# Performance work log

Measured on AMD Instinct MI355X. Metric: run time of the kernel, lower is better.

The kernel has to match this reference:

```python
import jax, jax.numpy as jnp
import numpy as np
from jax import lax

DIM = 384
NUM_HEADS = 6
STRIDE_Q = 1
STRIDE_KV = 2
BN_EPS = 1e-5
SCALE = DIM ** (-0.5)  # CvT scales by dim_out, not head_dim


def setup_inputs() -> dict:
    key = jax.random.key(0)
    ks = jax.random.split(key, 8)
    B, H, W, C = 32, 28, 28, DIM
    T = 1 + H * W
    x = jax.random.normal(ks[0], (B, T, C), dtype=jnp.float32)
    conv_w = jax.random.normal(ks[1], (3, C, 1, 3, 3), dtype=jnp.float32) * 0.1
    bn_gamma = jnp.ones((3, C), dtype=jnp.float32)
    bn_beta = jnp.zeros((3, C), dtype=jnp.float32)
    bn_mean = jnp.zeros((3, C), dtype=jnp.float32)
    bn_var = jnp.ones((3, C), dtype=jnp.float32)
    w_q = jax.random.normal(ks[2], (C, C), dtype=jnp.float32) * 0.02
    w_k = jax.random.normal(ks[3], (C, C), dtype=jnp.float32) * 0.02
    w_v = jax.random.normal(ks[4], (C, C), dtype=jnp.float32) * 0.02
    w_proj = jax.random.normal(ks[5], (C, C), dtype=jnp.float32) * 0.02
    b_proj = jnp.zeros((C,), dtype=jnp.float32)
    return {"x": x, "conv_w": conv_w, "bn_gamma": bn_gamma, "bn_beta": bn_beta,
            "bn_mean": bn_mean, "bn_var": bn_var, "w_q": w_q, "w_k": w_k,
            "w_v": w_v, "w_proj": w_proj, "b_proj": b_proj, "h": H, "w": W}


def _dw_conv_bn(x_sp, cw, gamma, beta, mean, var, stride):
    # x_sp: [B, C, H, W]; cw: [C, 1, 3, 3] depthwise (groups=C); inference BN
    C = x_sp.shape[1]
    y = lax.conv_general_dilated(
        x_sp, cw, window_strides=(stride, stride), padding=((1, 1), (1, 1)),
        feature_group_count=C, dimension_numbers=("NCHW", "OIHW", "NCHW"))
    inv = gamma * lax.rsqrt(var + BN_EPS)
    y = y * inv[None, :, None, None] + (beta - mean * inv)[None, :, None, None]
    B, Cc, Hc, Wc = y.shape
    return y.reshape(B, Cc, Hc * Wc).transpose(0, 2, 1)  # b (h w) c


def reference(x, conv_w, bn_gamma, bn_beta, bn_mean, bn_var,
              w_q, w_k, w_v, w_proj, b_proj, h, w):
    B, T, C = x.shape
    nh, hd = NUM_HEADS, C // NUM_HEADS
    cls_tok, x_tok = x[:, :1], x[:, 1:]
    x_sp = x_tok.reshape(B, h, w, C).transpose(0, 3, 1, 2)  # b c h w

    q = _dw_conv_bn(x_sp, conv_w[0], bn_gamma[0], bn_beta[0], bn_mean[0], bn_var[0], STRIDE_Q)
    k = _dw_conv_bn(x_sp, conv_w[1], bn_gamma[1], bn_beta[1], bn_mean[1], bn_var[1], STRIDE_KV)
    v = _dw_conv_bn(x_sp, conv_w[2], bn_gamma[2], bn_beta[2], bn_mean[2], bn_var[2], STRIDE_KV)

    q = jnp.concatenate([cls_tok, q], axis=1)
    k = jnp.concatenate([cls_tok, k], axis=1)
    v = jnp.concatenate([cls_tok, v], axis=1)

    def split_heads(t, wm):  # linear proj then b t (h d) -> b h t d
        t = t @ wm.T
        Bt, Tt, _ = t.shape
        return t.reshape(Bt, Tt, nh, hd).transpose(0, 2, 1, 3)

    q = split_heads(q, w_q)
    k = split_heads(k, w_k)
    v = split_heads(v, w_v)

    attn = jax.nn.softmax(jnp.einsum("bhld,bhtd->bhlt", q, k) * SCALE, axis=-1)
    out = jnp.einsum("bhlt,bhtd->bhld", attn, v)
    out = out.transpose(0, 2, 1, 3).reshape(B, -1, C)  # b t (h d)
    return out @ w_proj.T + b_proj
```

## Files before the change

kernel.cpp:

```cpp
#include <hip/hip_runtime.h>
#include <math.h>

#define B_SZ   32
#define C_DIM  384
#define H_IN   28
#define W_IN   28
#define TQ     785
#define TKV    197
#define NH     6
#define HD     64
#define SCALE_F 0.05103103630798287f
#define SCALE_L2E (0.05103103630798287f * 1.4426950408889634f)
#define BN_EPS_F 1e-5f

#define QROWS    25120
#define KVROWS   6304
#define QROWS_P  25344
#define KVROWS_P 6528
#define WELEM    147456
#define VT_LD    208

#define QT256    99
#define KVT256   25

typedef _Float16 f16;
typedef f16  f16x8 __attribute__((ext_vector_type(8)));
typedef f16  f16x4 __attribute__((ext_vector_type(4)));
typedef float f32x4 __attribute__((ext_vector_type(4)));

__device__ __forceinline__ void split16(float v, f16& h, f16& l) {
    h = (f16)v;
    l = (f16)(v - (float)h);
}

__device__ __forceinline__ void cp16(void* lds, const void* g) {
    __builtin_amdgcn_global_load_lds(
        (const __attribute__((address_space(1))) unsigned int*)g,
        (__attribute__((address_space(3))) unsigned int*)lds, 16, 0, 0);
}

__device__ __forceinline__ bool swz(int id, int yMax, int& y, int& n0) {
    int g = id / 24, w = id - g * 24;
    y = g * 8 + (w & 7);
    n0 = (w >> 3) * 128;
    return y < yMax;
}

__global__ __launch_bounds__(256) void prep_kernel(
    const float* __restrict__ wq, const float* __restrict__ wk,
    const float* __restrict__ wv, const float* __restrict__ wp,
    const float* __restrict__ conv_w,
    const float* __restrict__ gamma, const float* __restrict__ beta,
    const float* __restrict__ mean, const float* __restrict__ var,
    f16* __restrict__ Wh, f16* __restrict__ Wl,
    float* __restrict__ wAll)
{
    int idx = blockIdx.x * 256 + threadIdx.x;
    if (idx < 4 * WELEM) {
        int which = idx / WELEM, rem = idx - which * WELEM;
        const float* s = (which == 0) ? wq : (which == 1) ? wk : (which == 2) ? wv : wp;
        float v = s[rem];
        if (which == 0) v *= SCALE_L2E;
        f16 h, l;
        split16(v, h, l);
        Wh[idx] = h; Wl[idx] = l;
    } else if (idx < 4 * WELEM + 3 * C_DIM) {
        int k = idx - 4 * WELEM;
        int cv = k / C_DIM, c = k - cv * C_DIM;
        float inv = gamma[k] * rsqrtf(var[k] + BN_EPS_F);
#pragma unroll
        for (int t = 0; t < 9; ++t)
            wAll[cv * 3840 + t * C_DIM + c] = conv_w[(size_t)cv * C_DIM * 9 + c * 9 + t] * inv;
        wAll[cv * 3840 + 9 * C_DIM + c] = beta[k] - mean[k] * inv;
    }
}

__global__ __launch_bounds__(256) void fused_conv_kernel(
    const float* __restrict__ x,
    const float* __restrict__ wAll,
    f16* __restrict__ q, f16* __restrict__ k, f16* __restrict__ v)
{
    __shared__ float sW[3 * 3840];
    int tid = threadIdx.x;
    int b = blockIdx.x, oi = blockIdx.y;

    if (oi == H_IN) {
        if (tid < 96) {
            int c = tid * 4;
            float4 vv = *(const float4*)&x[(size_t)b * TQ * C_DIM + c];
            float a[4] = {vv.x, vv.y, vv.z, vv.w};
            f16x4 hv;
#pragma unroll
            for (int u = 0; u < 4; ++u) hv[u] = (f16)a[u];
            size_t oq = (size_t)b * TQ * C_DIM + c;
            size_t okv = (size_t)b * TKV * C_DIM + c;
            *(f16x4*)&q[oq] = hv;
            *(f16x4*)&k[okv] = hv;
            *(f16x4*)&v[okv] = hv;
        }
        return;
    }

#pragma unroll
    for (int i = 0; i < 12; ++i) {
        int idx = tid + 256 * i;
        if (idx < 2880) cp16(&sW[idx * 4], &wAll[idx * 4]);
    }
    __syncthreads();

    const size_t xb = (size_t)b * TQ * C_DIM + C_DIM;
    bool oi_even = (oi & 1) == 0;

    for (int it = 0; it < 11; ++it) {
        int idx = tid + 256 * it;
        if (idx >= 28 * 96) break;
        int oj = idx / 96, cg = idx - oj * 96;
        int c = cg * 4;

        float4 xv[9];
#pragma unroll
        for (int di = 0; di < 3; ++di) {
            int ii = oi + di - 1;
            bool rok = (ii >= 0) && (ii < H_IN);
#pragma unroll
            for (int dj = 0; dj < 3; ++dj) {
                int jj = oj + dj - 1;
                bool ok = rok && (jj >= 0) && (jj < W_IN);
                xv[di * 3 + dj] = ok ? *(const float4*)&x[xb + ((size_t)ii * W_IN + jj) * C_DIM + c]
                                     : make_float4(0.f, 0.f, 0.f, 0.f);
            }
        }

        {
            float4 acc = *(const float4*)&sW[0 * 3840 + 9 * C_DIM + c];
#pragma unroll
            for (int t = 0; t < 9; ++t) {
                float4 w4 = *(const float4*)&sW[0 * 3840 + t * C_DIM + c];
                acc.x += w4.x * xv[t].x; acc.y += w4.y * xv[t].y;
                acc.z += w4.z * xv[t].z; acc.w += w4.w * xv[t].w;
            }
            f16x4 hv;
            hv[0] = (f16)acc.x; hv[1] = (f16)acc.y; hv[2] = (f16)acc.z; hv[3] = (f16)acc.w;
            size_t off = ((size_t)b * TQ + 1 + oi * W_IN + oj) * C_DIM + c;
            *(f16x4*)&q[off] = hv;
        }

        if (oi_even && ((oj & 1) == 0)) {
            int p = (oi >> 1) * 14 + (oj >> 1);
            size_t off = ((size_t)b * TKV + 1 + p) * C_DIM + c;
#pragma unroll
            for (int cv = 1; cv <= 2; ++cv) {
                float4 acc = *(const float4*)&sW[cv * 3840 + 9 * C_DIM + c];
#pragma unroll
                for (int t = 0; t < 9; ++t) {
                    float4 w4 = *(const float4*)&sW[cv * 3840 + t * C_DIM + c];
                    acc.x += w4.x * xv[t].x; acc.y += w4.y * xv[t].y;
                    acc.z += w4.z * xv[t].z; acc.w += w4.w * xv[t].w;
                }
                f16x4 hv;
                hv[0] = (f16)acc.x; hv[1] = (f16)acc.y; hv[2] = (f16)acc.z; hv[3] = (f16)acc.w;
                if (cv == 1) *(f16x4*)&k[off] = hv;
                else         *(f16x4*)&v[off] = hv;
            }
        }
    }
}

__device__ __forceinline__ void gemm_body_s(
    const f16* __restrict__ Ah,
    const f16* __restrict__ Wh, const f16* __restrict__ Wl,
    const float* __restrict__ bias,
    float* __restrict__ Cf, f16* __restrict__ Co,
    int M, int mode, int m0, int n0)
{
    __shared__ f16 lds[3 * 16384];

    const int t = threadIdx.x;
    const int wv = t >> 6, lane = t & 63;
    const int wr = (wv >> 1) * 64;
    const int wc = (wv & 1) * 64;
    const int lrow = lane & 15, quad = lane >> 4;
    const int qsw = quad ^ ((lrow >> 1) & 3);

    const int sr = t >> 2;
    const int g  = (t & 3) ^ ((t >> 3) & 3);

    const f16* gA0 = Ah + (size_t)(m0 + sr) * 384 + g * 8;
    const f16* gA1 = gA0 + 128 * 384;
    const f16* gBh = Wh + (size_t)(n0 + sr) * 384 + g * 8;
    const f16* gBl = Wl + (size_t)(n0 + sr) * 384 + g * 8;

#define STAGE_S(buf, kk) do {                                 \
        f16* d = lds + (buf) * 16384 + t * 8;                 \
        const int ko = (kk) * 32;                             \
        cp16(d,         gA0 + ko);                            \
        cp16(d + 4096,  gA1 + ko);                            \
        cp16(d + 8192,  gBh + ko);                            \
        cp16(d + 12288, gBl + ko);                            \
    } while (0)

    f32x4 acc[4][4];
#pragma unroll
    for (int i = 0; i < 4; ++i)
#pragma unroll
        for (int j = 0; j < 4; ++j)
            acc[i][j] = (f32x4){0.f, 0.f, 0.f, 0.f};

    STAGE_S(0, 0);
    STAGE_S(1, 1);

#pragma unroll
    for (int kk = 0; kk < 12; ++kk) {
        if (kk == 11) asm volatile("s_waitcnt vmcnt(0)" ::: "memory");
        else          asm volatile("s_waitcnt vmcnt(4)" ::: "memory");
        __builtin_amdgcn_s_barrier();
        __builtin_amdgcn_sched_barrier(0);

        if (kk < 10) {
            STAGE_S((kk + 2) % 3, kk + 2);
            __builtin_amdgcn_sched_barrier(0);
        }

        const f16* bp = lds + (kk % 3) * 16384;
        f16x8 ah[4], bh[4], bl[4];
#pragma unroll
        for (int i = 0; i < 4; ++i) {
            int ro = (wr + i * 16 + lrow) * 32 + qsw * 8;
            ah[i] = *(const f16x8*)&bp[ro];
        }
#pragma unroll
        for (int j = 0; j < 4; ++j) {
            int ro = (wc + j * 16 + lrow) * 32 + qsw * 8;
            bh[j] = *(const f16x8*)&bp[8192 + ro];
            bl[j] = *(const f16x8*)&bp[12288 + ro];
        }
        asm volatile("s_waitcnt lgkmcnt(0)" ::: "memory");
        __builtin_amdgcn_sched_barrier(0);

        __builtin_amdgcn_s_setprio(1);
#pragma unroll
        for (int i = 0; i < 4; ++i)
#pragma unroll
            for (int j = 0; j < 4; ++j) {
                acc[i][j] = __builtin_amdgcn_mfma_f32_16x16x32_f16(ah[i], bh[j], acc[i][j], 0, 0, 0);
                acc[i][j] = __builtin_amdgcn_mfma_f32_16x16x32_f16(ah[i], bl[j], acc[i][j], 0, 0, 0);
            }
        __builtin_amdgcn_s_setprio(0);
    }
#undef STAGE_S

#pragma unroll
    for (int i = 0; i < 4; ++i) {
        int grow0 = m0 + wr + i * 16 + quad * 4;
#pragma unroll
        for (int j = 0; j < 4; ++j) {
            int gcol = n0 + wc + j * 16 + lrow;
            float bb = (bias && mode == 0) ? bias[gcol] : 0.f;
#pragma unroll
            for (int r = 0; r < 4; ++r) {
                int grow = grow0 + r;
                if (grow >= M) continue;
                float vv = acc[i][j][r] + bb;
                if (mode == 0) {
                    Cf[(size_t)grow * 384 + gcol] = vv;
                } else if (mode == 1) {
                    Co[(size_t)grow * 384 + gcol] = (f16)vv;
                } else {
                    int bb2 = grow / TKV;
                    int key = grow - bb2 * TKV;
                    size_t off = (size_t)bb2 * 384 * VT_LD + (size_t)gcol * VT_LD + key;
                    Co[off] = (f16)vv;
                }
            }
        }
    }
}

__global__ __launch_bounds__(512, 2) void qkv_proj_kernel(
    const f16* __restrict__ q, const f16* __restrict__ k, const f16* __restrict__ v,
    const f16* __restrict__ Wh, const f16* __restrict__ Wl,
    f16* __restrict__ Qp, f16* __restrict__ Kp, f16* __restrict__ VT,
    int yMax)
{
    int y, n0;
    if (!swz(blockIdx.x, yMax, y, n0)) return;
    if (y < QT256)
        gemm_body_s(q, Wh, Wl, nullptr, nullptr, Qp, QROWS, 1, y * 256, n0);
    else if (y < QT256 + KVT256)
        gemm_body_s(k, Wh + WELEM, Wl + WELEM, nullptr, nullptr, Kp,
                    KVROWS, 1, (y - QT256) * 256, n0);
    else
        gemm_body_s(v, Wh + 2 * WELEM, Wl + 2 * WELEM, nullptr, nullptr, VT,
                    KVROWS, 2, (y - QT256 - KVT256) * 256, n0);
}

__global__ __launch_bounds__(512, 2) void v_proj_kernel(
    const f16* __restrict__ v,
    const f16* __restrict__ Wh, const f16* __restrict__ Wl,
    f16* __restrict__ VT)
{
    int y, n0;
    if (!swz(blockIdx.x, KVT256, y, n0)) return;
    gemm_body_s(v, Wh, Wl, nullptr, nullptr, VT, KVROWS, 2, y * 256, n0);
}

__global__ __launch_bounds__(512, 2) void out_proj_kernel(
    const f16* __restrict__ Ah,
    const f16* __restrict__ Wh, const f16* __restrict__ Wl,
    const float* __restrict__ bias, float* __restrict__ Cf)
{
    int y, n0;
    if (!swz(blockIdx.x, QT256, y, n0)) return;
    gemm_body_s(Ah, Wh, Wl, bias, Cf, nullptr, QROWS, 0, y * 256, n0);
}

__global__ __launch_bounds__(256) void attn_mfma8(
    const f16* __restrict__ Qp, const f16* __restrict__ Kp,
    const f16* __restrict__ VT, f16* __restrict__ Oh)
{
    __shared__ f16 sQ[2][64][32];
    __shared__ f16 sKa[2][64][32];
    __shared__ f16 sKb[2][64][32];
    __shared__ float sPs[64][68];

    int t = threadIdx.x;
    int wv = t >> 6, lane = t & 63;
    int c = lane & 15, quad = lane >> 4;
    int wq0 = wv * 16;

    int L = blockIdx.x;
    int xcd = L & 7, s_ = L >> 3;
    int pg = s_ / 13, tt = s_ - pg * 13;
    int panel = pg * 8 + xcd;
    int b = panel / NH, h = panel - b * NH;
    int q0 = tt * 64;

    const size_t qbase  = (size_t)b * TQ * C_DIM + h * HD;
    const size_t kbase  = (size_t)b * TKV * C_DIM + h * HD;
    const size_t vtbase = (size_t)b * 384 * VT_LD + (size_t)h * HD * VT_LD;

#define STAGE_T(DST, EXPR) do {                                      \
        _Pragma("unroll") for (int i = 0; i < 2; ++i) {              \
            int idx = t + 256 * i;                                   \
            int ks = idx >> 8, row = (idx >> 2) & 63, sg = (idx & 3) * 8; \
            cp16(&DST[ks][row][sg], (EXPR));                         \
        } } while (0)

#define QK(KT, BUF) do {                                             \
        __builtin_amdgcn_s_setprio(1);                               \
        _Pragma("unroll") for (int ks = 0; ks < 2; ++ks) {           \
            _Pragma("unroll") for (int j = 0; j < 4; ++j) {          \
                f16x8 k8 = *(const f16x8*)&BUF[ks][j * 16 + c][quad * 8]; \
                s[KT][j] = __builtin_amdgcn_mfma_f32_16x16x32_f16(q8[ks], k8, s[KT][j], 0, 0, 0); \
            } }                                                      \
        __builtin_amdgcn_s_setprio(0);                               \
    } while (0)

    f32x4 s[4][4];
#pragma unroll
    for (int kt = 0; kt < 4; ++kt)
#pragma unroll
        for (int j = 0; j < 4; ++j)
            s[kt][j] = (f32x4){0.f, 0.f, 0.f, 0.f};

    STAGE_T(sQ,  &Qp[qbase + (size_t)(q0 + row) * C_DIM + ks * 32 + sg]);
    STAGE_T(sKa, &Kp[kbase + (size_t)(0 * 64 + row) * C_DIM + ks * 32 + sg]);
    __syncthreads();

    f16x8 q8[2];
#pragma unroll
    for (int ks = 0; ks < 2; ++ks)
        q8[ks] = *(const f16x8*)&sQ[ks][wq0 + c][quad * 8];

    STAGE_T(sKb, &Kp[kbase + (size_t)(1 * 64 + row) * C_DIM + ks * 32 + sg]);
    QK(0, sKa);
    __syncthreads();
    STAGE_T(sKa, &Kp[kbase + (size_t)(2 * 64 + row) * C_DIM + ks * 32 + sg]);
    QK(1, sKb);
    __syncthreads();
    STAGE_T(sKb, &Kp[kbase + (size_t)(3 * 64 + row) * C_DIM + ks * 32 + sg]);
    QK(2, sKa);
    __syncthreads();
    QK(3, sKb);
    __syncthreads();

    STAGE_T(sKa, &VT[vtbase + (size_t)row * VT_LD + 0 * 64 + ks * 32 + sg]);
    STAGE_T(sKb, &VT[vtbase + (size_t)row * VT_LD + 1 * 64 + ks * 32 + sg]);

#pragma unroll
    for (int r = 0; r < 4; ++r) {
        s[3][0][r] = (c < 5) ? s[3][0][r] : -1e30f;
        s[3][1][r] = -1e30f;
        s[3][2][r] = -1e30f;
        s[3][3][r] = -1e30f;
    }

    float inv_r[4];
#pragma unroll
    for (int r = 0; r < 4; ++r) {
        float mx = -1e30f;
#pragma unroll
        for (int kt = 0; kt < 4; ++kt)
#pragma unroll
            for (int j = 0; j < 4; ++j)
                mx = fmaxf(mx, s[kt][j][r]);
        mx = fmaxf(mx, __shfl_xor(mx, 1));
        mx = fmaxf(mx, __shfl_xor(mx, 2));
        mx = fmaxf(mx, __shfl_xor(mx, 4));
        mx = fmaxf(mx, __shfl_xor(mx, 8));
        float sum = 0.f;
#pragma unroll
        for (int kt = 0; kt < 4; ++kt)
#pragma unroll
            for (int j = 0; j < 4; ++j) {
                float pv = exp2f(s[kt][j][r] - mx);
                s[kt][j][r] = pv;
                sum += pv;
            }
        sum += __shfl_xor(sum, 1);
        sum += __shfl_xor(sum, 2);
        sum += __shfl_xor(sum, 4);
        sum += __shfl_xor(sum, 8);
        inv_r[r] = 1.f / sum;
    }

    f32x4 o[4];
#pragma unroll
    for (int j = 0; j < 4; ++j) o[j] = (f32x4){0.f, 0.f, 0.f, 0.f};

#define SPS_WRITE(VTI) do {                                          \
        _Pragma("unroll") for (int r = 0; r < 4; ++r)                \
            _Pragma("unroll") for (int j = 0; j < 4; ++j)            \
                sPs[wq0 + quad * 4 + r][j * 16 + c] = s[VTI][j][r];  \
    } while (0)

#define PV(BUF) do {                                                 \
        _Pragma("unroll") for (int ks = 0; ks < 2; ++ks) {           \
            float4 p0 = *(const float4*)&sPs[wq0 + c][ks * 32 + quad * 8]; \
            float4 p1 = *(const float4*)&sPs[wq0 + c][ks * 32 + quad * 8 + 4]; \
            f16x8 p8;                                                \
            p8[0] = (f16)p0.x; p8[1] = (f16)p0.y; p8[2] = (f16)p0.z; p8[3] = (f16)p0.w; \
            p8[4] = (f16)p1.x; p8[5] = (f16)p1.y; p8[6] = (f16)p1.z; p8[7] = (f16)p1.w; \
            __builtin_amdgcn_s_setprio(1);                           \
            _Pragma("unroll") for (int j = 0; j < 4; ++j) {          \
                f16x8 v8 = *(const f16x8*)&BUF[ks][j * 16 + c][quad * 8]; \
                o[j] = __builtin_amdgcn_mfma_f32_16x16x32_f16(p8, v8, o[j], 0, 0, 0); \
            }                                                        \
            __builtin_amdgcn_s_setprio(0);                           \
        } } while (0)

    __syncthreads();
    SPS_WRITE(0);
    PV(sKa);
    __syncthreads();
    STAGE_T(sKa, &VT[vtbase + (size_t)row * VT_LD + 2 * 64 + ks * 32 + sg]);
    SPS_WRITE(1);
    PV(sKb);
    __syncthreads();
    STAGE_T(sKb, &VT[vtbase + (size_t)row * VT_LD + 3 * 64 + ks * 32 + sg]);
    SPS_WRITE(2);
    PV(sKa);
    __syncthreads();
    SPS_WRITE(3);
    PV(sKb);

#pragma unroll
    for (int r = 0; r < 4; ++r) {
        int gq = q0 + wq0 + quad * 4 + r;
        if (gq >= TQ) continue;
        float inv = inv_r[r];
#pragma unroll
        for (int j = 0; j < 4; ++j) {
            size_t off = (size_t)(b * TQ + gq) * C_DIM + h * HD + j * 16 + c;
            Oh[off] = (f16)(o[j][r] * inv);
        }
    }
#undef STAGE_T
#undef QK
#undef SPS_WRITE
#undef PV
}

extern "C" void kernel_launch(void* const* d_in, const int* in_sizes, int n_in,
                              void* d_out, int out_size, void* d_ws, size_t ws_size,
                              hipStream_t stream) {
    const float* x       = (const float*)d_in[0];
    const float* conv_w  = (const float*)d_in[1];
    const float* bn_g    = (const float*)d_in[2];
    const float* bn_b    = (const float*)d_in[3];
    const float* bn_m    = (const float*)d_in[4];
    const float* bn_v    = (const float*)d_in[5];
    const float* w_q     = (const float*)d_in[6];
    const float* w_k     = (const float*)d_in[7];
    const float* w_v     = (const float*)d_in[8];
    const float* w_proj  = (const float*)d_in[9];
    const float* b_proj  = (const float*)d_in[10];
    float* out = (float*)d_out;

    const size_t QS    = (size_t)QROWS_P * 384 * sizeof(f16);
    const size_t KVS   = (size_t)KVROWS_P * 384 * sizeof(f16);
    const size_t WSZ   = 4 * (size_t)WELEM * sizeof(f16);
    const size_t VTS   = (size_t)B_SZ * 384 * VT_LD * sizeof(f16);
    const size_t WALLS = 3 * 3840 * sizeof(float);

    char* p = (char*)d_ws;
    f16* q   = (f16*)p; p += QS;
    f16* k   = (f16*)p; p += KVS;
    f16* v   = (f16*)p; p += KVS;
    f16* Wh  = (f16*)p; p += WSZ;
    f16* Wl  = (f16*)p; p += WSZ;
    f16* Qp  = (f16*)p; p += QS;
    f16* Kp  = (f16*)p; p += KVS;
    float* wAll = (float*)p; p += WALLS;

    size_t used = (size_t)(p - (char*)d_ws);
    bool sepVT = (ws_size >= used + VTS);
    f16* VT = sepVT ? (f16*)p : k;
    f16* oh = q;

    {
        int total = 4 * WELEM + 3 * C_DIM;
        prep_kernel<<<(total + 255) / 256, 256, 0, stream>>>(
            w_q, w_k, w_v, w_proj, conv_w, bn_g, bn_b, bn_m, bn_v, Wh, Wl, wAll);
    }

    {
        dim3 gc(B_SZ, H_IN + 1);
        fused_conv_kernel<<<gc, 256, 0, stream>>>(x, wAll, q, k, v);
    }

    if (sepVT) {
        int yMax = QT256 + 2 * KVT256;
        int nb = ((yMax + 7) / 8) * 24;
        qkv_proj_kernel<<<nb, 512, 0, stream>>>(q, k, v, Wh, Wl, Qp, Kp, VT, yMax);
    } else {
        int yMax = QT256 + KVT256;
        int nb = ((yMax + 7) / 8) * 24;
        qkv_proj_kernel<<<nb, 512, 0, stream>>>(q, k, v, Wh, Wl, Qp, Kp, VT, yMax);
        int nbv = ((KVT256 + 7) / 8) * 24;
        v_proj_kernel<<<nbv, 512, 0, stream>>>(v, Wh + 2 * WELEM, Wl + 2 * WELEM, VT);
    }

    {
        attn_mfma8<<<2496, 256, 0, stream>>>(Qp, Kp, VT, oh);
    }

    {
        int nb = ((QT256 + 7) / 8) * 24;
        out_proj_kernel<<<nb, 512, 0, stream>>>(oh, Wh + 3 * WELEM, Wl + 3 * WELEM,
                                                b_proj, out);
    }
}
```

Before: 243.4 us.

## Retile projection GEMMs to full-width N rows with B read from global

The projection GEMMs switch from 256x128 tiles with both A and B staged in LDS to 128x384 tiles, where each block covers the full output width. Only A is staged in LDS, and the high/low weight fragments are loaded directly from global memory (expected to stay cache-resident) into registers. Each A tile is now read once instead of three times, and the block-swizzle mapping is dropped. In exchange, every wave issues many uncoalesced global loads for B each k-step, and it holds 24 accumulators per wave, which raises register pressure.

```diff
diff --git a/kernel.cpp b/kernel.cpp
--- a/kernel.cpp
+++ b/kernel.cpp
@@ -20,8 +20,8 @@
 #define WELEM    147456
 #define VT_LD    208
 
-#define QT256    99
-#define KVT256   25
+#define QT128    198
+#define KVT128   51
 
 typedef _Float16 f16;
 typedef f16  f16x8 __attribute__((ext_vector_type(8)));
@@ -37,13 +37,6 @@
     __builtin_amdgcn_global_load_lds(
         (const __attribute__((address_space(1))) unsigned int*)g,
         (__attribute__((address_space(3))) unsigned int*)lds, 16, 0, 0);
-}
-
-__device__ __forceinline__ bool swz(int id, int yMax, int& y, int& n0) {
-    int g = id / 24, w = id - g * 24;
-    y = g * 8 + (w & 7);
-    n0 = (w >> 3) * 128;
-    return y < yMax;
 }
 
 __global__ __launch_bounds__(256) void prep_kernel(
@@ -166,74 +159,66 @@
     }
 }
 
-__device__ __forceinline__ void gemm_body_s(
+__device__ __forceinline__ void gemm_body8(
     const f16* __restrict__ Ah,
     const f16* __restrict__ Wh, const f16* __restrict__ Wl,
     const float* __restrict__ bias,
     float* __restrict__ Cf, f16* __restrict__ Co,
-    int M, int mode, int m0, int n0)
-{
-    __shared__ f16 lds[3 * 16384];
+    int M, int mode, int m0)
+{
+    __shared__ f16 lds[3 * 4096];
 
     const int t = threadIdx.x;
     const int wv = t >> 6, lane = t & 63;
-    const int wr = (wv >> 1) * 64;
-    const int wc = (wv & 1) * 64;
+    const int wr = (wv >> 2) * 64;
+    const int wc = (wv & 3) * 96;
     const int lrow = lane & 15, quad = lane >> 4;
     const int qsw = quad ^ ((lrow >> 1) & 3);
 
     const int sr = t >> 2;
     const int g  = (t & 3) ^ ((t >> 3) & 3);
-
-    const f16* gA0 = Ah + (size_t)(m0 + sr) * 384 + g * 8;
-    const f16* gA1 = gA0 + 128 * 384;
-    const f16* gBh = Wh + (size_t)(n0 + sr) * 384 + g * 8;
-    const f16* gBl = Wl + (size_t)(n0 + sr) * 384 + g * 8;
-
-#define STAGE_S(buf, kk) do {                                 \
-        f16* d = lds + (buf) * 16384 + t * 8;                 \
-        const int ko = (kk) * 32;                             \
-        cp16(d,         gA0 + ko);                            \
-        cp16(d + 4096,  gA1 + ko);                            \
-        cp16(d + 8192,  gBh + ko);                            \
-        cp16(d + 12288, gBl + ko);                            \
-    } while (0)
-
-    f32x4 acc[4][4];
+    const f16* gA = Ah + (size_t)(m0 + sr) * 384 + g * 8;
+
+    const f16* pBh[6];
+    const f16* pBl[6];
+#pragma unroll
+    for (int j = 0; j < 6; ++j) {
+        pBh[j] = Wh + (size_t)(wc + j * 16 + lrow) * 384 + quad * 8;
+        pBl[j] = Wl + (size_t)(wc + j * 16 + lrow) * 384 + quad * 8;
+    }
+
+#define STAGE_A(buf, kk) cp16(lds + (buf) * 4096 + t * 8, gA + (kk) * 32)
+
+    f32x4 acc[4][6];
 #pragma unroll
     for (int i = 0; i < 4; ++i)
 #pragma unroll
-        for (int j = 0; j < 4; ++j)
+        for (int j = 0; j < 6; ++j)
             acc[i][j] = (f32x4){0.f, 0.f, 0.f, 0.f};
 
-    STAGE_S(0, 0);
-    STAGE_S(1, 1);
+    STAGE_A(0, 0);
+    STAGE_A(1, 1);
 
 #pragma unroll
     for (int kk = 0; kk < 12; ++kk) {
         if (kk == 11) asm volatile("s_waitcnt vmcnt(0)" ::: "memory");
-        else          asm volatile("s_waitcnt vmcnt(4)" ::: "memory");
+        else          asm volatile("s_waitcnt vmcnt(1)" ::: "memory");
         __builtin_amdgcn_s_barrier();
-        __builtin_amdgcn_sched_barrier(0);
-
-        if (kk < 10) {
-            STAGE_S((kk + 2) % 3, kk + 2);
-            __builtin_amdgcn_sched_barrier(0);
-        }
-
-        const f16* bp = lds + (kk % 3) * 16384;
-        f16x8 ah[4], bh[4], bl[4];
-#pragma unroll
-        for (int i = 0; i < 4; ++i) {
-            int ro = (wr + i * 16 + lrow) * 32 + qsw * 8;
-            ah[i] = *(const f16x8*)&bp[ro];
-        }
-#pragma unroll
-        for (int j = 0; j < 4; ++j) {
-            int ro = (wc + j * 16 + lrow) * 32 + qsw * 8;
-            bh[j] = *(const f16x8*)&bp[8192 + ro];
-            bl[j] = *(const f16x8*)&bp[12288 + ro];
-        }
+
+        if (kk < 10) STAGE_A((kk + 2) % 3, kk + 2);
+
+        f16x8 bh[6], bl[6];
+#pragma unroll
+        for (int j = 0; j < 6; ++j) {
+            bh[j] = *(const f16x8*)(pBh[j] + kk * 32);
+            bl[j] = *(const f16x8*)(pBl[j] + kk * 32);
+        }
+
+        const f16* bp = lds + (kk % 3) * 4096;
+        f16x8 ah[4];
+#pragma unroll
+        for (int i = 0; i < 4; ++i)
+            ah[i] = *(const f16x8*)&bp[(wr + i * 16 + lrow) * 32 + qsw * 8];
         asm volatile("s_waitcnt lgkmcnt(0)" ::: "memory");
         __builtin_amdgcn_sched_barrier(0);
 
@@ -241,20 +226,20 @@
 #pragma unroll
         for (int i = 0; i < 4; ++i)
 #pragma unroll
-            for (int j = 0; j < 4; ++j) {
+            for (int j = 0; j < 6; ++j) {
                 acc[i][j] = __builtin_amdgcn_mfma_f32_16x16x32_f16(ah[i], bh[j], acc[i][j], 0, 0, 0);
                 acc[i][j] = __builtin_amdgcn_mfma_f32_16x16x32_f16(ah[i], bl[j], acc[i][j], 0, 0, 0);
             }
         __builtin_amdgcn_s_setprio(0);
     }
-#undef STAGE_S
+#undef STAGE_A
 
 #pragma unroll
     for (int i = 0; i < 4; ++i) {
         int grow0 = m0 + wr + i * 16 + quad * 4;
 #pragma unroll
-        for (int j = 0; j < 4; ++j) {
-            int gcol = n0 + wc + j * 16 + lrow;
+        for (int j = 0; j < 6; ++j) {
+            int gcol = wc + j * 16 + lrow;
             float bb = (bias && mode == 0) ? bias[gcol] : 0.f;
 #pragma unroll
             for (int r = 0; r < 4; ++r) {
@@ -282,16 +267,16 @@
     f16* __restrict__ Qp, f16* __restrict__ Kp, f16* __restrict__ VT,
     int yMax)
 {
-    int y, n0;
-    if (!swz(blockIdx.x, yMax, y, n0)) return;
-    if (y < QT256)
-        gemm_body_s(q, Wh, Wl, nullptr, nullptr, Qp, QROWS, 1, y * 256, n0);
-    else if (y < QT256 + KVT256)
-        gemm_body_s(k, Wh + WELEM, Wl + WELEM, nullptr, nullptr, Kp,
-                    KVROWS, 1, (y - QT256) * 256, n0);
+    int y = blockIdx.x;
+    if (y >= yMax) return;
+    if (y < QT128)
+        gemm_body8(q, Wh, Wl, nullptr, nullptr, Qp, QROWS, 1, y * 128);
+    else if (y < QT128 + KVT128)
+        gemm_body8(k, Wh + WELEM, Wl + WELEM, nullptr, nullptr, Kp,
+                   KVROWS, 1, (y - QT128) * 128);
     else
-        gemm_body_s(v, Wh + 2 * WELEM, Wl + 2 * WELEM, nullptr, nullptr, VT,
-                    KVROWS, 2, (y - QT256 - KVT256) * 256, n0);
+        gemm_body8(v, Wh + 2 * WELEM, Wl + 2 * WELEM, nullptr, nullptr, VT,
+                   KVROWS, 2, (y - QT128 - KVT128) * 128);
 }
 
 __global__ __launch_bounds__(512, 2) void v_proj_kernel(
@@ -299,9 +284,9 @@
     const f16* __restrict__ Wh, const f16* __restrict__ Wl,
     f16* __restrict__ VT)
 {
-    int y, n0;
-    if (!swz(blockIdx.x, KVT256, y, n0)) return;
-    gemm_body_s(v, Wh, Wl, nullptr, nullptr, VT, KVROWS, 2, y * 256, n0);
+    int y = blockIdx.x;
+    if (y >= KVT128) return;
+    gemm_body8(v, Wh, Wl, nullptr, nullptr, VT, KVROWS, 2, y * 128);
 }
 
 __global__ __launch_bounds__(512, 2) void out_proj_kernel(
@@ -309,9 +294,9 @@
     const f16* __restrict__ Wh, const f16* __restrict__ Wl,
     const float* __restrict__ bias, float* __restrict__ Cf)
 {
-    int y, n0;
-    if (!swz(blockIdx.x, QT256, y, n0)) return;
-    gemm_body_s(Ah, Wh, Wl, bias, Cf, nullptr, QROWS, 0, y * 256, n0);
+    int y = blockIdx.x;
+    if (y >= QT128) return;
+    gemm_body8(Ah, Wh, Wl, bias, Cf, nullptr, QROWS, 0, y * 128);
 }
 
 __global__ __launch_bounds__(256) void attn_mfma8(
@@ -530,15 +515,12 @@
     }
 
     if (sepVT) {
-        int yMax = QT256 + 2 * KVT256;
-        int nb = ((yMax + 7) / 8) * 24;
-        qkv_proj_kernel<<<nb, 512, 0, stream>>>(q, k, v, Wh, Wl, Qp, Kp, VT, yMax);
+        int yMax = QT128 + 2 * KVT128;
+        qkv_proj_kernel<<<yMax, 512, 0, stream>>>(q, k, v, Wh, Wl, Qp, Kp, VT, yMax);
     } else {
-        int yMax = QT256 + KVT256;
-        int nb = ((yMax + 7) / 8) * 24;
-        qkv_proj_kernel<<<nb, 512, 0, stream>>>(q, k, v, Wh, Wl, Qp, Kp, VT, yMax);
-        int nbv = ((KVT256 + 7) / 8) * 24;
-        v_proj_kernel<<<nbv, 512, 0, stream>>>(v, Wh + 2 * WELEM, Wl + 2 * WELEM, VT);
+        int yMax = QT128 + KVT128;
+        qkv_proj_kernel<<<yMax, 512, 0, stream>>>(q, k, v, Wh, Wl, Qp, Kp, VT, yMax);
+        v_proj_kernel<<<KVT128, 512, 0, stream>>>(v, Wh + 2 * WELEM, Wl + 2 * WELEM, VT);
     }
 
     {
@@ -546,8 +528,7 @@
     }
 
     {
-        int nb = ((QT256 + 7) / 8) * 24;
-        out_proj_kernel<<<nb, 512, 0, stream>>>(oh, Wh + 3 * WELEM, Wl + 3 * WELEM,
-                                                b_proj, out);
-    }
-}
+        out_proj_kernel<<<QT128, 512, 0, stream>>>(oh, Wh + 3 * WELEM, Wl + 3 * WELEM,
+                                                   b_proj, out);
+    }
+}
```

Result: slower. 325.7 us (+33.8%).
